# Optimization experiments

Measured on AMD Instinct MI355X. Metric: run time of the kernel, lower is better.

Reference implementation:

```python
import jax, jax.numpy as jnp
import numpy as np

B, DIM, H, W = 2, 192, 256, 256
WIN = 4
EPS = 1e-5


def _cd_conj(x):
    if len(x) == 1:
        return x
    h = len(x) // 2
    return np.concatenate([_cd_conj(x[:h]), -x[h:]])


def _cd_mult(a, b):
    n = len(a)
    if n == 1:
        return a * b
    h = n // 2
    a1, a2, b1, b2 = a[:h], a[h:], b[:h], b[h:]
    c1 = _cd_mult(a1, b1) - _cd_mult(_cd_conj(b2), a2)
    c2 = _cd_mult(b2, a1) + _cd_mult(a2, _cd_conj(b1))
    return np.concatenate([c1, c2])


def _sedenion_table(n=16):
    # M[i, j, k] = sign s such that e_i * e_j = s * e_k (Cayley-Dickson)
    eye = np.eye(n, dtype=np.float32)
    M = np.zeros((n, n, n), dtype=np.float32)
    for i in range(n):
        for j in range(n):
            M[i, j] = _cd_mult(eye[i], eye[j])
    return M

SED_TABLE = jnp.asarray(_sedenion_table(16))  # (16,16,16)


def layer_norm(x, g, b):
    m = x.mean(-1, keepdims=True)
    v = ((x - m) ** 2).mean(-1, keepdims=True)
    return (x - m) * jax.lax.rsqrt(v + EPS) * g + b


def get_window(x):
    # (B,C,H,W) -> (B,H/4,W/4, s1*s2*C)
    b, c, h, w = x.shape
    x = x.reshape(b, c, h // WIN, WIN, w // WIN, WIN)
    x = x.transpose(0, 2, 4, 3, 5, 1)  # b, h', w', s1, s2, c
    return x.reshape(b, h // WIN, w // WIN, WIN * WIN * c)


def reverse_window(x, c):
    b, hh, ww, _ = x.shape
    x = x.reshape(b, hh, ww, WIN, WIN, c)
    x = x.transpose(0, 5, 1, 3, 2, 4)  # b, c, h', s1, w', s2
    return x.reshape(b, c, hh * WIN, ww * WIN)


def sedenion_full_weight(w_sed):
    # w_sed: (16, dim, dim) component weights -> (16*dim, 16*dim) structured matrix
    d = w_sed.shape[1]
    wf = jnp.einsum('ijk,jde->idke', SED_TABLE, w_sed)
    return wf.reshape(16 * d, 16 * w_sed.shape[2])


def setup_inputs() -> dict:
    key = jax.random.key(0)
    ks = jax.random.split(key, 8)
    d, dh = DIM, 4 * DIM
    s = 0.02
    return {
        'x': jax.random.normal(ks[0], (B, DIM, H, W), jnp.float32),
        'norm1_g': jnp.ones((d,), jnp.float32),
        'norm1_b': jnp.zeros((d,), jnp.float32),
        'w_sed': jax.random.normal(ks[1], (16, d, d), jnp.float32) * s,
        'proj_w': jax.random.normal(ks[2], (d, d), jnp.float32) * s,
        'proj_b': jnp.zeros((d,), jnp.float32),
        'norm2_g': jnp.ones((d,), jnp.float32),
        'norm2_b': jnp.zeros((d,), jnp.float32),
        'fc1_w': jax.random.normal(ks[3], (d, dh), jnp.float32) * s,
        'fc1_b': jnp.zeros((dh,), jnp.float32),
        'fc2_w': jax.random.normal(ks[4], (dh, d), jnp.float32) * s,
        'fc2_b': jnp.zeros((d,), jnp.float32),
    }


def reference(x, norm1_g, norm1_b, w_sed, proj_w, proj_b,
              norm2_g, norm2_b, fc1_w, fc1_b, fc2_w, fc2_b):
    b, c, h, w = x.shape
    # --- attention branch (norm1 -> window -> sedenion linear -> unwindow -> gelu -> proj) ---
    xn = layer_norm(x.transpose(0, 2, 3, 1), norm1_g, norm1_b).transpose(0, 3, 1, 2)
    xw = get_window(xn)                               # (B, H/4, W/4, 16*C)
    wf = sedenion_full_weight(w_sed)                  # (16C, 16C)
    xw = xw @ wf
    x1 = reverse_window(xw, c)                        # (B, C, H, W)
    y = x1.transpose(0, 2, 3, 1)                      # b h w c
    y = jax.nn.gelu(y, approximate=False)
    y = y @ proj_w + proj_b
    x = x + y.transpose(0, 3, 1, 2)
    # --- mlp branch ---
    hbr = layer_norm(x.transpose(0, 2, 3, 1), norm2_g, norm2_b)
    hbr = jax.nn.gelu(hbr @ fc1_w + fc1_b, approximate=False)
    hbr = hbr @ fc2_w + fc2_b
    x = x + hbr.transpose(0, 3, 1, 2)
    return x
```

## Files before the change

kernel.cpp:

```cpp
#include <hip/hip_runtime.h>

typedef short short8 __attribute__((ext_vector_type(8)));
typedef float f32x4 __attribute__((ext_vector_type(4)));

#define DEVINL __device__ __forceinline__

struct SedTab { signed char s[256]; unsigned char j[256]; };

static void cd_mult_host(const float* a, const float* b, float* r, int n) {
    if (n == 1) { r[0] = a[0] * b[0]; return; }
    int h = n / 2;
    float cb1[8], cb2[8], t1[8], t2[8], t3[8], t4[8];
    cb1[0] = b[0]; for (int i = 1; i < h; ++i) cb1[i] = -b[i];
    cb2[0] = b[h]; for (int i = 1; i < h; ++i) cb2[i] = -b[h + i];
    cd_mult_host(a,     b,   t1, h);
    cd_mult_host(cb2,   a+h, t2, h);
    cd_mult_host(b+h,   a,   t3, h);
    cd_mult_host(a+h,   cb1, t4, h);
    for (int i = 0; i < h; ++i) { r[i] = t1[i] - t2[i]; r[h + i] = t3[i] + t4[i]; }
}

static SedTab build_sed() {
    SedTab t{};
    for (int i = 0; i < 16; ++i)
        for (int jj = 0; jj < 16; ++jj) {
            float a[16] = {0}, b[16] = {0}, r[16] = {0};
            a[i] = 1.0f; b[jj] = 1.0f;
            cd_mult_host(a, b, r, 16);
            for (int k = 0; k < 16; ++k)
                if (r[k] != 0.0f) {
                    t.s[i * 16 + k] = (r[k] > 0.f) ? 1 : -1;
                    t.j[i * 16 + k] = (unsigned char)jj;
                }
        }
    return t;
}
static const SedTab g_sed = build_sed();

DEVINL unsigned short f2bf(float v) {
    union { float f; unsigned int u; } c; c.f = v;
    unsigned int r = (c.u + 0x7FFFu + ((c.u >> 16) & 1u)) >> 16;
    return (unsigned short)r;
}
DEVINL float bf2f(unsigned short u) {
    union { unsigned int i; float f; } c; c.i = ((unsigned int)u) << 16; return c.f;
}

DEVINL float gelu_f(float v) {
    float u = 1.5957691216f * (v + 0.044715f * v * v * v);
    return v * __builtin_amdgcn_rcpf(1.0f + __expf(-u));
}

DEVINL void gl2lds16(const void* g, void* l) {
    __builtin_amdgcn_global_load_lds((__attribute__((address_space(1))) const unsigned int*)g,
                                     (__attribute__((address_space(3))) unsigned int*)l, 16, 0, 0);
}

DEVINL int swz(int k, int row) {
    return (k & ~63) | ((((k >> 3) ^ row) & 7) << 3) | (k & 7);
}

__global__ __launch_bounds__(256) void build_wft(const float* __restrict__ w_sed,
                                                 unsigned short* __restrict__ wfT,
                                                 SedTab tab) {
    __shared__ float t[32][33];
    int n0 = blockIdx.y * 32, kk0 = blockIdx.x * 32;
    int k = n0 / 192, i = kk0 / 192;
    int j = tab.j[i * 16 + k];
    float s = (float)tab.s[i * 16 + k];
    int e0 = n0 - k * 192, dd0 = kk0 - i * 192;
    int tx = threadIdx.x & 31, ty = threadIdx.x >> 5;
    const float* base = w_sed + ((size_t)j * 192 + dd0) * 192 + e0;
    for (int it = 0; it < 4; ++it) {
        int row = ty + it * 8;
        t[row][tx] = base[(size_t)row * 192 + tx];
    }
    __syncthreads();
    unsigned short* ob = wfT + (size_t)n0 * 3072 + kk0;
    for (int it = 0; it < 4; ++it) {
        int row = ty + it * 8;
        ob[(size_t)row * 3072 + tx] = f2bf(s * t[tx][row]);
    }
}

__global__ __launch_bounds__(256) void prep_w(const float* __restrict__ proj,
                                              const float* __restrict__ fc1,
                                              const float* __restrict__ fc2,
                                              unsigned short* __restrict__ projT,
                                              unsigned short* __restrict__ fc1T,
                                              unsigned short* __restrict__ fc2T) {
    int t = blockIdx.x * 256 + threadIdx.x;
    if (t < 192 * 192) projT[t] = f2bf(proj[(t % 192) * 192 + t / 192]);
    if (t < 768 * 192) {
        int n = t / 192, k = t % 192;
        fc1T[n * 192 + swz(k, n)] = f2bf(fc1[(size_t)k * 768 + n]);
    }
    if (t < 192 * 768) {
        int o = t / 768, k = t % 768;
        fc2T[o * 768 + swz(k, o)] = f2bf(fc2[(size_t)k * 192 + o]);
    }
}

__global__ __launch_bounds__(256) void ln1_win(const float* __restrict__ x,
                                               const float* __restrict__ g,
                                               const float* __restrict__ bta,
                                               unsigned short* __restrict__ xw,
                                               unsigned short* __restrict__ xwin) {
    __shared__ float vals[192 * 65];
    __shared__ float ps[8][64];
    __shared__ float mrs[2][64];
    int t = threadIdx.x;
    int bid = blockIdx.x;
    int x0 = (bid & 3) << 6;
    int y  = (bid >> 2) & 255;
    int b  = bid >> 10;
    int px = t & 63, cg = t >> 6;
    const float* xp = x + ((size_t)b * 192 * 65536) + (size_t)y * 256 + x0 + px;
    float s = 0.f, s2 = 0.f;
    for (int c = cg; c < 192; c += 4) {
        float v = xp[(size_t)c * 65536];
        vals[c * 65 + px] = v;
        s += v; s2 += v * v;
    }
    ps[cg][px] = s; ps[cg + 4][px] = s2;
    __syncthreads();
    if (t < 64) {
        float S  = ps[0][t] + ps[1][t] + ps[2][t] + ps[3][t];
        float S2 = ps[4][t] + ps[5][t] + ps[6][t] + ps[7][t];
        float mean = S * (1.0f / 192.0f);
        float var  = S2 * (1.0f / 192.0f) - mean * mean;
        mrs[0][t] = mean;
        mrs[1][t] = rsqrtf(var + 1e-5f);
    }
    __syncthreads();
    int wh = y >> 2, wr = y & 3;
    for (int i = t; i < 192 * 64; i += 256) {
        int p = i / 192;
        int c = i - p * 192;
        float v = vals[c * 65 + p];
        int xx = x0 + p;
        int ww = xx >> 2, wc = xx & 3;
        int gp = ((b * 64 + wh) * 64 + ww) * 16 + wr * 4 + wc;
        size_t o = (size_t)gp * 192 + c;
        xwin[o] = f2bf(v);
        xw[o] = f2bf((v - mrs[0][p]) * mrs[1][p] * g[c] + bta[c]);
    }
}

__global__ __launch_bounds__(256, 2) void gemm_fused(
        const unsigned short* __restrict__ A,
        const unsigned short* __restrict__ BT,
        const unsigned short* __restrict__ projTw,
        const float* __restrict__ pbias,
        unsigned short* __restrict__ outB,
        unsigned short* __restrict__ xresb,
        const float* __restrict__ g2, const float* __restrict__ b2) {
    constexpr int K = 3072;
    __shared__ __align__(16) char smem[73728];
    short* lsA = (short*)smem;
    short* lsB = (short*)(smem + 16384);
    short* A2t = (short*)smem;
    short* lsP = (short*)(smem + 49152);
    int tid = threadIdx.x, lane = tid & 63, wid = tid >> 6;
    int wrow = wid >> 1, wcol = wid & 1;
    int lm = lane & 15, lq = lane >> 4;
    int bm = blockIdx.x * 128;
    int by = blockIdx.y;
    const unsigned short* Ag = A + (size_t)bm * K;
    const unsigned short* Bg = BT + (size_t)by * 192 * K;
    f32x4 acc[4][6] = {};
    for (int k0 = 0; k0 < K; k0 += 64) {
        #pragma unroll
        for (int it = 0; it < 4; ++it) {
            int p = (it * 4 + wid) * 64 + lane;
            int r = p >> 3;
            int q = (p & 7) ^ (r & 7);
            gl2lds16(Ag + (size_t)r * K + k0 + q * 8, lsA + (it * 4 + wid) * 512);
        }
        #pragma unroll
        for (int it = 0; it < 6; ++it) {
            int p = (it * 4 + wid) * 64 + lane;
            int r = p >> 3;
            int q = (p & 7) ^ (r & 7);
            gl2lds16(Bg + (size_t)r * K + k0 + q * 8, lsB + (it * 4 + wid) * 512);
        }
        __syncthreads();
        #pragma unroll
        for (int s = 0; s < 2; ++s) {
            short8 af[4], bfr[6];
            #pragma unroll
            for (int mt = 0; mt < 4; ++mt) {
                int r = wrow * 64 + mt * 16 + lm;
                int q = s * 4 + lq;
                int pos = r * 8 + (q ^ (r & 7));
                af[mt] = *(const short8*)&lsA[pos * 8];
            }
            #pragma unroll
            for (int nt = 0; nt < 6; ++nt) {
                int r = wcol * 96 + nt * 16 + lm;
                int q = s * 4 + lq;
                int pos = r * 8 + (q ^ (r & 7));
                bfr[nt] = *(const short8*)&lsB[pos * 8];
            }
            #pragma unroll
            for (int mt = 0; mt < 4; ++mt)
                #pragma unroll
                for (int nt = 0; nt < 6; ++nt)
                    acc[mt][nt] = __builtin_amdgcn_mfma_f32_16x16x32_bf16(af[mt], bfr[nt], acc[mt][nt], 0, 0, 0);
        }
        __syncthreads();
    }
    #pragma unroll
    for (int mt = 0; mt < 4; ++mt)
        #pragma unroll
        for (int nt = 0; nt < 6; ++nt)
            #pragma unroll
            for (int r = 0; r < 4; ++r) {
                int row = wrow * 64 + mt * 16 + lq * 4 + r;
                int c = wcol * 96 + nt * 16 + lm;
                A2t[row * 192 + swz(c, row)] = f2bf(gelu_f(acc[mt][nt][r]));
            }
    #pragma unroll
    for (int mt = 0; mt < 4; ++mt)
        #pragma unroll
        for (int nt = 0; nt < 6; ++nt)
            acc[mt][nt] = f32x4{0.f, 0.f, 0.f, 0.f};
    __syncthreads();
    for (int k0 = 0; k0 < 192; k0 += 64) {
        #pragma unroll
        for (int it = 0; it < 6; ++it) {
            int p = (it * 4 + wid) * 64 + lane;
            int r = p >> 3;
            int q = (p & 7) ^ (r & 7);
            gl2lds16(projTw + (size_t)r * 192 + k0 + q * 8, lsP + (it * 4 + wid) * 512);
        }
        __syncthreads();
        #pragma unroll
        for (int s = 0; s < 2; ++s) {
            short8 af[4], bfr[6];
            #pragma unroll
            for (int mt = 0; mt < 4; ++mt) {
                int r = wrow * 64 + mt * 16 + lm;
                int cg = (k0 >> 3) + s * 4 + lq;
                int slot = (cg & ~7) | ((cg ^ r) & 7);
                af[mt] = *(const short8*)&A2t[r * 192 + slot * 8];
            }
            #pragma unroll
            for (int nt = 0; nt < 6; ++nt) {
                int r = wcol * 96 + nt * 16 + lm;
                int q = s * 4 + lq;
                int pos = r * 8 + (q ^ (r & 7));
                bfr[nt] = *(const short8*)&lsP[pos * 8];
            }
            #pragma unroll
            for (int mt = 0; mt < 4; ++mt)
                #pragma unroll
                for (int nt = 0; nt < 6; ++nt)
                    acc[mt][nt] = __builtin_amdgcn_mfma_f32_16x16x32_bf16(af[mt], bfr[nt], acc[mt][nt], 0, 0, 0);
        }
        __syncthreads();
    }
    float sA[4][4], s2A[4][4];
    #pragma unroll
    for (int mt = 0; mt < 4; ++mt)
        #pragma unroll
        for (int r = 0; r < 4; ++r) { sA[mt][r] = 0.f; s2A[mt][r] = 0.f; }
    #pragma unroll
    for (int mt = 0; mt < 4; ++mt)
        #pragma unroll
        for (int nt = 0; nt < 6; ++nt)
            #pragma unroll
            for (int r = 0; r < 4; ++r) {
                int rl = wrow * 64 + mt * 16 + lq * 4 + r;
                int gc = wcol * 96 + nt * 16 + lm;
                size_t gp = (size_t)(bm + rl) * 16 + by;
                size_t o = gp * 192 + gc;
                float v = bf2f(xresb[o]) + acc[mt][nt][r] + pbias[gc];
                xresb[o] = f2bf(v);
                acc[mt][nt][r] = v;
                sA[mt][r] += v; s2A[mt][r] += v * v;
            }
    #pragma unroll
    for (int mt = 0; mt < 4; ++mt)
        #pragma unroll
        for (int r = 0; r < 4; ++r)
            #pragma unroll
            for (int msk = 1; msk < 16; msk <<= 1) {
                sA[mt][r]  += __shfl_xor(sA[mt][r],  msk, 64);
                s2A[mt][r] += __shfl_xor(s2A[mt][r], msk, 64);
            }
    float* psS   = (float*)smem;
    float* psS2  = psS + 256;
    float* pmean = psS2 + 256;
    float* prsig = pmean + 128;
    if (lm == 0) {
        #pragma unroll
        for (int mt = 0; mt < 4; ++mt)
            #pragma unroll
            for (int r = 0; r < 4; ++r) {
                int rl = wrow * 64 + mt * 16 + lq * 4 + r;
                psS [rl * 2 + wcol] = sA[mt][r];
                psS2[rl * 2 + wcol] = s2A[mt][r];
            }
    }
    __syncthreads();
    if (tid < 128) {
        float S  = psS[tid * 2]  + psS[tid * 2 + 1];
        float S2 = psS2[tid * 2] + psS2[tid * 2 + 1];
        float mean = S * (1.0f / 192.0f);
        float var  = S2 * (1.0f / 192.0f) - mean * mean;
        pmean[tid] = mean;
        prsig[tid] = rsqrtf(var + 1e-5f);
    }
    __syncthreads();
    float gw[6], bw[6];
    #pragma unroll
    for (int nt = 0; nt < 6; ++nt) {
        int gc = wcol * 96 + nt * 16 + lm;
        gw[nt] = g2[gc]; bw[nt] = b2[gc];
    }
    #pragma unroll
    for (int mt = 0; mt < 4; ++mt)
        #pragma unroll
        for (int nt = 0; nt < 6; ++nt)
            #pragma unroll
            for (int r = 0; r < 4; ++r) {
                int rl = wrow * 64 + mt * 16 + lq * 4 + r;
                int gc = wcol * 96 + nt * 16 + lm;
                int gp = (bm + rl) * 16 + by;
                float v = (acc[mt][nt][r] - pmean[rl]) * prsig[rl] * gw[nt] + bw[nt];
                outB[(size_t)gp * 192 + swz(gc, gp)] = f2bf(v);
            }
}

__global__ __launch_bounds__(512, 2) void ffn_fused(
        const unsigned short* __restrict__ A3, const unsigned short* __restrict__ fc1T,
        const unsigned short* __restrict__ fc2T, const float* __restrict__ b1,
        const float* __restrict__ b2, const unsigned short* __restrict__ xresb,
        float* __restrict__ outF) {
    __shared__ __align__(16) char smem[65536];
    short* wA = (short*)smem;
    short* wB = (short*)(smem + 24576);
    short* Sb = (short*)(smem + 49152);
    int tid = threadIdx.x, lane = tid & 63, wid = tid >> 6;
    int wrow = wid >> 1, wcol = wid & 1;
    int lm = lane & 15, lq = lane >> 4;
    int bm = blockIdx.x * 128;

    const unsigned short* A3g = A3 + (size_t)bm * 192;

    auto stage_fc1 = [&](int slice) {
        const unsigned short* f1g = fc1T + (size_t)slice * 64 * 192;
        #pragma unroll
        for (int it = 0; it < 3; ++it) {
            int cb = it * 512 + wid * 64;
            gl2lds16(f1g + (size_t)(cb + lane) * 8, wA + cb * 8);
        }
    };
    auto stage_fc2 = [&](int slice) {
        int kb = slice * 64;
        #pragma unroll
        for (int it = 0; it < 3; ++it) {
            int cb = it * 512 + wid * 64;
            int ch = cb + lane;
            gl2lds16(fc2T + (size_t)(ch >> 3) * 768 + kb + (ch & 7) * 8, wB + cb * 8);
        }
    };

    stage_fc1(0);
    stage_fc2(0);

    short8 af[6][2];
    #pragma unroll
    for (int ks = 0; ks < 6; ++ks) {
        int c = ks * 4 + lq;
        #pragma unroll
        for (int mt = 0; mt < 2; ++mt) {
            int r = wrow * 32 + mt * 16 + lm;
            int slot = (c & ~7) | ((c ^ r) & 7);
            af[ks][mt] = *(const short8*)&A3g[(size_t)r * 192 + slot * 8];
        }
    }
    __syncthreads();

    f32x4 acc2[2][6] = {};
    for (int nb = 0; nb < 12; ++nb) {
        f32x4 acc1[2][2] = {};
        __builtin_amdgcn_s_setprio(1);
        #pragma unroll
        for (int ks = 0; ks < 6; ++ks) {
            int c = ks * 4 + lq;
            short8 bfr[2];
            #pragma unroll
            for (int nt = 0; nt < 2; ++nt) {
                int n = wcol * 32 + nt * 16 + lm;
                int slot = (c & ~7) | ((c ^ n) & 7);
                bfr[nt] = *(const short8*)&wA[n * 192 + slot * 8];
            }
            #pragma unroll
            for (int mt = 0; mt < 2; ++mt)
                #pragma unroll
                for (int nt = 0; nt < 2; ++nt)
                    acc1[mt][nt] = __builtin_amdgcn_mfma_f32_16x16x32_bf16(af[ks][mt], bfr[nt], acc1[mt][nt], 0, 0, 0);
        }
        __builtin_amdgcn_s_setprio(0);
        #pragma unroll
        for (int nt = 0; nt < 2; ++nt) {
            int cl = wcol * 32 + nt * 16 + lm;
            float bv = b1[nb * 64 + cl];
            #pragma unroll
            for (int mt = 0; mt < 2; ++mt)
                #pragma unroll
                for (int r = 0; r < 4; ++r) {
                    int row = wrow * 32 + mt * 16 + lq * 4 + r;
                    float v = gelu_f(acc1[mt][nt][r] + bv);
                    int slot = ((cl >> 3) ^ row) & 7;
                    Sb[row * 64 + slot * 8 + (cl & 7)] = f2bf(v);
                }
        }
        asm volatile("s_waitcnt vmcnt(0) lgkmcnt(0)" ::: "memory");
        __builtin_amdgcn_sched_barrier(0);
        __builtin_amdgcn_s_barrier();
        __builtin_amdgcn_sched_barrier(0);
        if (nb < 11) stage_fc1(nb + 1);
        __builtin_amdgcn_s_setprio(1);
        #pragma unroll
        for (int ks = 0; ks < 2; ++ks) {
            int c = ks * 4 + lq;
            short8 sf[2], wf[6];
            #pragma unroll
            for (int mt = 0; mt < 2; ++mt) {
                int r = wrow * 32 + mt * 16 + lm;
                int slot = (c ^ r) & 7;
                sf[mt] = *(const short8*)&Sb[r * 64 + slot * 8];
            }
            #pragma unroll
            for (int nt = 0; nt < 6; ++nt) {
                int o = wcol * 96 + nt * 16 + lm;
                int slot = (c ^ o) & 7;
                wf[nt] = *(const short8*)&wB[o * 64 + slot * 8];
            }
            #pragma unroll
            for (int mt = 0; mt < 2; ++mt)
                #pragma unroll
                for (int nt = 0; nt < 6; ++nt)
                    acc2[mt][nt] = __builtin_amdgcn_mfma_f32_16x16x32_bf16(sf[mt], wf[nt], acc2[mt][nt], 0, 0, 0);
        }
        __builtin_amdgcn_s_setprio(0);
        asm volatile("s_waitcnt vmcnt(0) lgkmcnt(0)" ::: "memory");
        __builtin_amdgcn_sched_barrier(0);
        __builtin_amdgcn_s_barrier();
        __builtin_amdgcn_sched_barrier(0);
        if (nb < 11) stage_fc2(nb + 1);
    }
    float* T = (float*)smem;
    #pragma unroll
    for (int pass = 0; pass < 2; ++pass) {
        if ((wrow >> 1) == pass) {
            #pragma unroll
            for (int nt = 0; nt < 6; ++nt) {
                int col = wcol * 96 + nt * 16 + lm;
                float bv = b2[col];
                #pragma unroll
                for (int mt = 0; mt < 2; ++mt)
                    #pragma unroll
                    for (int r = 0; r < 4; ++r) {
                        int row = wrow * 32 + mt * 16 + lq * 4 + r;
                        int rowT = row - pass * 64;
                        float xr = bf2f(xresb[(size_t)(bm + row) * 192 + col]);
                        T[rowT * 201 + col] = acc2[mt][nt][r] + bv + xr;
                    }
            }
        }
        __syncthreads();
        int bmg = bm + pass * 64;
        int b  = bmg >> 16;
        int wh = (bmg >> 10) & 63;
        int ww0 = (bmg >> 4) & 63;
        int ybase = wh * 4, xbase = ww0 * 4;
        for (int idx = tid; idx < 3072; idx += 512) {
            int xq = idx & 3, run = idx >> 2;
            int c = run >> 2, wr = run & 3;
            int p = xq * 16 + wr * 4;
            f32x4 val;
            val[0] = T[(p + 0) * 201 + c];
            val[1] = T[(p + 1) * 201 + c];
            val[2] = T[(p + 2) * 201 + c];
            val[3] = T[(p + 3) * 201 + c];
            size_t o = (((size_t)b * 192 + c) * 256 + (ybase + wr)) * 256 + xbase + xq * 4;
            *(f32x4*)&outF[o] = val;
        }
        __syncthreads();
    }
}

extern "C" void kernel_launch(void* const* d_in, const int* in_sizes, int n_in,
                              void* d_out, int out_size, void* d_ws, size_t ws_size,
                              hipStream_t stream) {
    const float* x      = (const float*)d_in[0];
    const float* n1g    = (const float*)d_in[1];
    const float* n1b    = (const float*)d_in[2];
    const float* w_sed  = (const float*)d_in[3];
    const float* proj_w = (const float*)d_in[4];
    const float* proj_b = (const float*)d_in[5];
    const float* n2g    = (const float*)d_in[6];
    const float* n2b    = (const float*)d_in[7];
    const float* fc1_w  = (const float*)d_in[8];
    const float* fc1_b  = (const float*)d_in[9];
    const float* fc2_w  = (const float*)d_in[10];
    const float* fc2_b  = (const float*)d_in[11];
    float* out = (float*)d_out;

    char* ws = (char*)d_ws;
    unsigned short* wfT   = (unsigned short*)(ws);
    unsigned short* xw    = (unsigned short*)(ws + 18874368);
    unsigned short* A3    = (unsigned short*)(ws + 69206016);
    unsigned short* xresb = (unsigned short*)(ws + 119537664);
    unsigned short* projT = (unsigned short*)(ws + 169869312);
    unsigned short* fc1T  = (unsigned short*)(ws + 169943040);
    unsigned short* fc2T  = (unsigned short*)(ws + 170237952);

    build_wft<<<dim3(96, 96), 256, 0, stream>>>(w_sed, wfT, g_sed);
    prep_w<<<576, 256, 0, stream>>>(proj_w, fc1_w, fc2_w, projT, fc1T, fc2T);
    ln1_win<<<2048, 256, 0, stream>>>(x, n1g, n1b, xw, xresb);

    gemm_fused<<<dim3(64, 16), 256, 0, stream>>>(
        xw, wfT, projT, proj_b, A3, xresb, n2g, n2b);
    ffn_fused<<<1024, 512, 0, stream>>>(A3, fc1T, fc2T, fc1_b, fc2_b, xresb, out);
}
```

Before: 576.2 us.

## Double-buffer K-loop in fused sedenion GEMM and swap grid block order

Replaces the single-buffered K=64 main loop of the sedenion GEMM with a double-buffered K=32 pipeline: the next tile is loaded into LDS while MFMAs run on the current one, with one barrier per step instead of two. The swizzle pattern is adjusted for 32-wide tiles. The grid is transposed so consecutive blocks share the same A row-block across N tiles, which is meant to improve L2 reuse of activations. Smaller K steps mean more barriers overall, and the full vmcnt(0) wait limits how much load latency can be hidden.

After: 605.5 us. 1.05x slower.

```diff
diff --git a/kernel.cpp b/kernel.cpp
--- a/kernel.cpp
+++ b/kernel.cpp
@@ -157,59 +157,77 @@
         const float* __restrict__ g2, const float* __restrict__ b2) {
     constexpr int K = 3072;
     __shared__ __align__(16) char smem[73728];
-    short* lsA = (short*)smem;
-    short* lsB = (short*)(smem + 16384);
+    short* lsA0 = (short*)smem;
+    short* lsB0 = (short*)(smem + 8192);
+    short* lsA1 = (short*)(smem + 20480);
+    short* lsB1 = (short*)(smem + 28672);
     short* A2t = (short*)smem;
     short* lsP = (short*)(smem + 49152);
     int tid = threadIdx.x, lane = tid & 63, wid = tid >> 6;
     int wrow = wid >> 1, wcol = wid & 1;
     int lm = lane & 15, lq = lane >> 4;
-    int bm = blockIdx.x * 128;
-    int by = blockIdx.y;
+    int by = blockIdx.x;
+    int bm = blockIdx.y * 128;
     const unsigned short* Ag = A + (size_t)bm * K;
     const unsigned short* Bg = BT + (size_t)by * 192 * K;
+
+    auto stage = [&](int t, short* dA, short* dB) {
+        int k0 = t * 32;
+        #pragma unroll
+        for (int it = 0; it < 2; ++it) {
+            int p = (it * 4 + wid) * 64 + lane;
+            int r = p >> 2, q = (p & 3) ^ (r & 3);
+            gl2lds16(Ag + (size_t)r * K + k0 + q * 8, dA + (it * 4 + wid) * 512);
+        }
+        #pragma unroll
+        for (int it = 0; it < 3; ++it) {
+            int p = (it * 4 + wid) * 64 + lane;
+            int r = p >> 2, q = (p & 3) ^ (r & 3);
+            gl2lds16(Bg + (size_t)r * K + k0 + q * 8, dB + (it * 4 + wid) * 512);
+        }
+    };
+
     f32x4 acc[4][6] = {};
-    for (int k0 = 0; k0 < K; k0 += 64) {
-        #pragma unroll
-        for (int it = 0; it < 4; ++it) {
-            int p = (it * 4 + wid) * 64 + lane;
-            int r = p >> 3;
-            int q = (p & 7) ^ (r & 7);
-            gl2lds16(Ag + (size_t)r * K + k0 + q * 8, lsA + (it * 4 + wid) * 512);
-        }
-        #pragma unroll
-        for (int it = 0; it < 6; ++it) {
-            int p = (it * 4 + wid) * 64 + lane;
-            int r = p >> 3;
-            int q = (p & 7) ^ (r & 7);
-            gl2lds16(Bg + (size_t)r * K + k0 + q * 8, lsB + (it * 4 + wid) * 512);
-        }
-        __syncthreads();
-        #pragma unroll
-        for (int s = 0; s < 2; ++s) {
-            short8 af[4], bfr[6];
-            #pragma unroll
-            for (int mt = 0; mt < 4; ++mt) {
-                int r = wrow * 64 + mt * 16 + lm;
-                int q = s * 4 + lq;
-                int pos = r * 8 + (q ^ (r & 7));
-                af[mt] = *(const short8*)&lsA[pos * 8];
-            }
-            #pragma unroll
-            for (int nt = 0; nt < 6; ++nt) {
-                int r = wcol * 96 + nt * 16 + lm;
-                int q = s * 4 + lq;
-                int pos = r * 8 + (q ^ (r & 7));
-                bfr[nt] = *(const short8*)&lsB[pos * 8];
-            }
-            #pragma unroll
-            for (int mt = 0; mt < 4; ++mt)
-                #pragma unroll
-                for (int nt = 0; nt < 6; ++nt)
-                    acc[mt][nt] = __builtin_amdgcn_mfma_f32_16x16x32_bf16(af[mt], bfr[nt], acc[mt][nt], 0, 0, 0);
-        }
-        __syncthreads();
-    }
+    auto compute = [&](const short* lA, const short* lB) {
+        short8 af[4], bfr[6];
+        #pragma unroll
+        for (int mt = 0; mt < 4; ++mt) {
+            int r = wrow * 64 + mt * 16 + lm;
+            int pos = r * 4 + (lq ^ (r & 3));
+            af[mt] = *(const short8*)&lA[pos * 8];
+        }
+        #pragma unroll
+        for (int nt = 0; nt < 6; ++nt) {
+            int r = wcol * 96 + nt * 16 + lm;
+            int pos = r * 4 + (lq ^ (r & 3));
+            bfr[nt] = *(const short8*)&lB[pos * 8];
+        }
+        #pragma unroll
+        for (int mt = 0; mt < 4; ++mt)
+            #pragma unroll
+            for (int nt = 0; nt < 6; ++nt)
+                acc[mt][nt] = __builtin_amdgcn_mfma_f32_16x16x32_bf16(af[mt], bfr[nt], acc[mt][nt], 0, 0, 0);
+    };
+
+    #define KSYNC() do { \
+        __builtin_amdgcn_sched_barrier(0); \
+        asm volatile("s_waitcnt vmcnt(0)" ::: "memory"); \
+        __builtin_amdgcn_sched_barrier(0); \
+        __builtin_amdgcn_s_barrier(); \
+        __builtin_amdgcn_sched_barrier(0); \
+    } while (0)
+
+    stage(0, lsA0, lsB0);
+    KSYNC();
+    for (int t = 0; t < 96; t += 2) {
+        stage(t + 1, lsA1, lsB1);
+        compute(lsA0, lsB0);
+        KSYNC();
+        if (t + 2 < 96) stage(t + 2, lsA0, lsB0);
+        compute(lsA1, lsB1);
+        KSYNC();
+    }
+    #undef KSYNC
     #pragma unroll
     for (int mt = 0; mt < 4; ++mt)
         #pragma unroll
@@ -524,7 +542,7 @@
     prep_w<<<576, 256, 0, stream>>>(proj_w, fc1_w, fc2_w, projT, fc1T, fc2T);
     ln1_win<<<2048, 256, 0, stream>>>(x, n1g, n1b, xw, xresb);
 
-    gemm_fused<<<dim3(64, 16), 256, 0, stream>>>(
+    gemm_fused<<<dim3(16, 64), 256, 0, stream>>>(
         xw, wfT, projT, proj_b, A3, xresb, n2g, n2b);
     ffn_fused<<<1024, 512, 0, stream>>>(A3, fc1T, fc2T, fc1_b, fc2_b, xresb, out);
 }
```
